# Performance work log

Hardware: AMD Instinct MI355X
Metric: run time of the kernel (lower is better)

## Reference

```python
import jax, jax.numpy as jnp
import numpy as np

L = 4          # num_layers
D = 512        # d_model
NH = 8         # num_heads
DH = 64        # d_head
DFF = 2048     # d_ff
EPS = 1e-5     # nn.LayerNorm default eps


def _layer_norm(x, g, b):
    m = x.mean(axis=-1, keepdims=True)
    v = ((x - m) ** 2).mean(axis=-1, keepdims=True)
    return (x - m) / jnp.sqrt(v + EPS) * g + b


def setup_inputs() -> dict:
    key = jax.random.key(0)
    ks = jax.random.split(key, 14)
    s = 0.02
    z = jax.random.normal(ks[0], (4, 16, D, 8, 8), dtype=jnp.float32)
    Wq = s * jax.random.normal(ks[1], (L, D, NH * DH), dtype=jnp.float32)
    Wk = s * jax.random.normal(ks[2], (L, D, NH * DH), dtype=jnp.float32)
    Wv = s * jax.random.normal(ks[3], (L, D, NH * DH), dtype=jnp.float32)
    Wo = s * jax.random.normal(ks[4], (L, NH * DH, D), dtype=jnp.float32)
    W1 = s * jax.random.normal(ks[5], (L, D, DFF), dtype=jnp.float32)
    b1 = jnp.zeros((L, DFF), dtype=jnp.float32)
    W2 = s * jax.random.normal(ks[6], (L, DFF, D), dtype=jnp.float32)
    b2 = jnp.zeros((L, D), dtype=jnp.float32)
    ln1_g = jnp.ones((L, D), dtype=jnp.float32)
    ln1_b = jnp.zeros((L, D), dtype=jnp.float32)
    ln2_g = jnp.ones((L, D), dtype=jnp.float32)
    ln2_b = jnp.zeros((L, D), dtype=jnp.float32)
    return {"z": z, "Wq": Wq, "Wk": Wk, "Wv": Wv, "Wo": Wo,
            "W1": W1, "b1": b1, "W2": W2, "b2": b2,
            "ln1_g": ln1_g, "ln1_b": ln1_b, "ln2_g": ln2_g, "ln2_b": ln2_b}


def _forward(z, Wq, Wk, Wv, Wo, W1, b1, W2, b2, ln1_g, ln1_b, ln2_g, ln2_b):
    B, T, Dm, H, W = z.shape
    N = H * W
    Tp = T * N  # T' = t*h*w
    # sinusoidal positional embedding over T' positions
    pos = jnp.arange(Tp, dtype=z.dtype)
    inv_freq = 1.0 / (10000.0 ** (jnp.arange(0, Dm, 2, dtype=z.dtype) / Dm))
    si = pos[:, None] * inv_freq[None, :]                 # (T', D/2)
    pos_emb = jnp.concatenate([jnp.sin(si), jnp.cos(si)], axis=-1)[:, None, :]  # (T',1,D)
    # rearrange 'b t d h w -> (t h w) b d'
    x = jnp.transpose(z, (1, 3, 4, 0, 2)).reshape(Tp, B, Dm)
    x = x + pos_emb
    # block-causal mask at block size N (True = masked)
    blk = jnp.arange(Tp) // N
    mask = blk[None, :] > blk[:, None]                    # (T'_q, T'_k)
    scale = 1.0 / np.sqrt(DH)
    outs = []
    for l in range(L):
        # post-lnorm multi-head attention (LN applied before residual add)
        q = (x @ Wq[l]).reshape(Tp, B, NH, DH)
        k = (x @ Wk[l]).reshape(Tp, B, NH, DH)
        v = (x @ Wv[l]).reshape(Tp, B, NH, DH)
        s = jnp.einsum('ibnd,jbnd->ijbn', q, k) * scale
        s = jnp.where(mask[:, :, None, None], -jnp.inf, s)
        p = jax.nn.softmax(s, axis=1)
        av = jnp.einsum('ijbn,jbnd->ibnd', p, v).reshape(Tp, B, NH * DH)
        attn = _layer_norm(av @ Wo[l], ln1_g[l], ln1_b[l])
        x = attn + x
        ff = _layer_norm(jax.nn.relu(x @ W1[l] + b1[l]) @ W2[l] + b2[l], ln2_g[l], ln2_b[l])
        x = ff + x
        outs.append(x)
    out = jnp.stack(outs, axis=1)                         # (T', L, B, D)
    # rearrange '(t h w) l b d -> b t l d h w'
    out = out.reshape(T, H, W, L, B, Dm)
    return jnp.transpose(out, (4, 0, 3, 5, 1, 2))


def reference(z, Wq, Wk, Wv, Wo, W1, b1, W2, b2, ln1_g, ln1_b, ln2_g, ln2_b):
    return _forward(z, Wq, Wk, Wv, Wo, W1, b1, W2, b2, ln1_g, ln1_b, ln2_g, ln2_b)
```

## Files before the change

### kernel.cpp

```cpp
#include <hip/hip_runtime.h>
#include <hip/hip_bf16.h>
#include <math.h>


#define TP 1024
#define BB 4
#define DD 512
#define DHEAD 64
#define DFF 2048
#define MROWS (TP*BB)
#define EPS 1e-5f
#define CSC 0.18033688011112042f

typedef __attribute__((ext_vector_type(8))) short bf16x8;
typedef __attribute__((ext_vector_type(4))) float f32x4;

__device__ __forceinline__ float b2f(unsigned short u) {
    union { unsigned int i; float f; } z; z.i = ((unsigned int)u) << 16; return z.f;
}
__device__ __forceinline__ unsigned short f2bu(float f) {
    __hip_bfloat16 h = __float2bfloat16(f);
    return *reinterpret_cast<unsigned short*>(&h);
}

#define WAITV0() asm volatile("s_waitcnt vmcnt(0)" ::: "memory")
#define WAITV4() asm volatile("s_waitcnt vmcnt(4)" ::: "memory")
#define WAITV8() asm volatile("s_waitcnt vmcnt(8)" ::: "memory")
#define WAITL0() asm volatile("s_waitcnt lgkmcnt(0)" ::: "memory")
__device__ __forceinline__ void hard_barrier() {
    __builtin_amdgcn_sched_barrier(0);
    __builtin_amdgcn_s_barrier();
    __builtin_amdgcn_sched_barrier(0);
}
__device__ __forceinline__ void waitv_ahead(int ahead) {
    if (ahead == 2) WAITV8();
    else if (ahead == 1) WAITV4();
    else WAITV0();
}
#define GLOAD(gp, lp) __builtin_amdgcn_global_load_lds( \
    (const __attribute__((address_space(1))) void*)(gp), \
    (__attribute__((address_space(3))) void*)(lp), 16, 0, 0)

__device__ __forceinline__ int fsw(int row) { return (row ^ (row >> 2)) & 3; }

__global__ __launch_bounds__(256) void embed_kernel(const float* __restrict__ z,
                                                    float* __restrict__ x,
                                                    __hip_bfloat16* __restrict__ x_bf) {
    __shared__ float tile[64][65];
    const int blk = blockIdx.x;
    const int dc = blk & 7, b = (blk >> 3) & 3, t = blk >> 5;
    const int tid = threadIdx.x;
#pragma unroll
    for (int it = 0; it < 4; ++it) {
        int idx = it * 256 + tid;
        int d_i = idx >> 4, hw4 = (idx & 15) * 4;
        int d = dc * 64 + d_i;
        float4 v = *reinterpret_cast<const float4*>(
            z + ((size_t)((b * 16 + t) * 512 + d)) * 64 + hw4);
        int j = d & 255;
        float freq = expf(-(float)(2 * j) * (9.210340371976184f / 512.0f));
        int i0 = t * 64 + hw4;
#pragma unroll
        for (int e = 0; e < 4; ++e) {
            float si = (float)(i0 + e) * freq;
            float pe = (d < 256) ? sinf(si) : cosf(si);
            tile[d_i][hw4 + e] = ((&v.x)[e]) + pe;
        }
    }
    __syncthreads();
#pragma unroll
    for (int it = 0; it < 4; ++it) {
        int idx = it * 256 + tid;
        int hw_o = idx >> 4, dq = (idx & 15) * 4;
        int row = (t * 64 + hw_o) * 4 + b;
        float4 v = make_float4(tile[dq][hw_o], tile[dq + 1][hw_o],
                               tile[dq + 2][hw_o], tile[dq + 3][hw_o]);
        *reinterpret_cast<float4*>(x + (size_t)row * 512 + dc * 64 + dq) = v;
        ushort4 u;
        u.x = f2bu(v.x); u.y = f2bu(v.y); u.z = f2bu(v.z); u.w = f2bu(v.w);
        *reinterpret_cast<ushort4*>((unsigned short*)x_bf + (size_t)row * 512 + dc * 64 + dq) = u;
    }
}

__global__ __launch_bounds__(256) void wt_convert(
    const float* __restrict__ Wq, const float* __restrict__ Wk,
    const float* __restrict__ Wv, const float* __restrict__ Wo,
    const float* __restrict__ W1, const float* __restrict__ W2,
    __hip_bfloat16* __restrict__ wall) {
    __shared__ float tile[32][33];
    const int l = blockIdx.y;
    __hip_bfloat16* wl = wall + (size_t)l * (4 * 512 * 512 + 2 * 512 * 2048);
    int b = blockIdx.x;
    const float* src; __hip_bfloat16* dst; int R, C, local, cbs;
    if (b < 1024) {
        int m = b >> 8; local = b & 255; R = 512; C = 512; cbs = 4;
        src = ((m == 0) ? Wq : (m == 1) ? Wk : (m == 2) ? Wv : Wo) + (size_t)l * 512 * 512;
        dst = wl + m * 512 * 512;
    } else if (b < 2048) {
        local = b - 1024; R = 512; C = 2048; cbs = 6;
        src = W1 + (size_t)l * 512 * 2048; dst = wl + 4 * 512 * 512;
    } else {
        local = b - 2048; R = 2048; C = 512; cbs = 4;
        src = W2 + (size_t)l * 2048 * 512; dst = wl + 4 * 512 * 512 + 512 * 2048;
    }
    int bx = local & ((1 << cbs) - 1), by = local >> cbs;
    int tx = threadIdx.x & 31, ty = threadIdx.x >> 5;
#pragma unroll
    for (int j = 0; j < 4; ++j)
        tile[ty + j * 8][tx] = src[(size_t)(by * 32 + ty + j * 8) * C + bx * 32 + tx];
    __syncthreads();
#pragma unroll
    for (int j = 0; j < 4; ++j)
        dst[(size_t)(bx * 32 + ty + j * 8) * R + by * 32 + tx] =
            __float2bfloat16(tile[tx][ty + j * 8]);
}

template<bool BIAS, bool RELU, bool OUT_BF16>
__global__ __launch_bounds__(256) void gemm_k(const __hip_bfloat16* __restrict__ A,
                                              const __hip_bfloat16* __restrict__ Bt,
                                              const float* __restrict__ bias,
                                              void* __restrict__ Cout,
                                              int N, int K, int ntx) {
    __shared__ __hip_bfloat16 As[4][128 * 32];
    __shared__ __hip_bfloat16 Bs[4][128 * 32];

    const int lb = blockIdx.x;
    const int wg = (lb & 7) * (gridDim.x >> 3) + (lb >> 3);
    const int m0 = (wg / ntx) * 128;
    const int n0 = (wg % ntx) * 128;

    const int tid  = threadIdx.x;
    const int wave = tid >> 6;
    const int lane = tid & 63;
    const int lr   = lane & 15;
    const int hi   = lane >> 4;
    const int lk   = (hi ^ fsw(lr)) << 3;
    const int wr   = (wave >> 1) * 64;
    const int wc   = (wave & 1) * 64;

    f32x4 acc[4][4];
#pragma unroll
    for (int i = 0; i < 4; ++i)
#pragma unroll
        for (int j = 0; j < 4; ++j) acc[i][j] = (f32x4){0.f, 0.f, 0.f, 0.f};

    const int c0 = tid, c1 = tid + 256;
    const __hip_bfloat16* a0 = A  + (size_t)(m0 + (c0 >> 2)) * K + (((c0 & 3) ^ fsw(c0 >> 2)) << 3);
    const __hip_bfloat16* a1 = A  + (size_t)(m0 + (c1 >> 2)) * K + (((c1 & 3) ^ fsw(c1 >> 2)) << 3);
    const __hip_bfloat16* b0 = Bt + (size_t)(n0 + (c0 >> 2)) * K + (((c0 & 3) ^ fsw(c0 >> 2)) << 3);
    const __hip_bfloat16* b1 = Bt + (size_t)(n0 + (c1 >> 2)) * K + (((c1 & 3) ^ fsw(c1 >> 2)) << 3);
    const int o0 = wave * 512, o1 = 2048 + wave * 512;

    const int nst = K >> 5;
#pragma unroll
    for (int s = 0; s < 3; ++s) {
        GLOAD(a0 + s * 32, &As[s][o0]); GLOAD(a1 + s * 32, &As[s][o1]);
        GLOAD(b0 + s * 32, &Bs[s][o0]); GLOAD(b1 + s * 32, &Bs[s][o1]);
    }

    for (int k = 0; k < nst; ++k) {
        const int ahead = (nst - 1 - k >= 2) ? 2 : (nst - 1 - k);
        waitv_ahead(ahead);
        hard_barrier();
        if (k + 3 < nst) {
            const int kk = (k + 3) << 5, bb = (k + 3) & 3;
            GLOAD(a0 + kk, &As[bb][o0]); GLOAD(a1 + kk, &As[bb][o1]);
            GLOAD(b0 + kk, &Bs[bb][o0]); GLOAD(b1 + kk, &Bs[bb][o1]);
        }
        const int buf = k & 3;
        bf16x8 af[4], bfv[4];
#pragma unroll
        for (int i = 0; i < 4; ++i)
            af[i] = *reinterpret_cast<const bf16x8*>(&As[buf][(size_t)(wr + i * 16 + lr) * 32 + lk]);
#pragma unroll
        for (int j = 0; j < 4; ++j)
            bfv[j] = *reinterpret_cast<const bf16x8*>(&Bs[buf][(size_t)(wc + j * 16 + lr) * 32 + lk]);
        __builtin_amdgcn_s_setprio(1);
#pragma unroll
        for (int i = 0; i < 4; ++i)
#pragma unroll
            for (int j = 0; j < 4; ++j)
                acc[i][j] = __builtin_amdgcn_mfma_f32_16x16x32_bf16(af[i], bfv[j], acc[i][j], 0, 0, 0);
        __builtin_amdgcn_s_setprio(0);
    }

#pragma unroll
    for (int j = 0; j < 4; ++j) {
        int col = n0 + wc + j * 16 + lr;
        float bv = BIAS ? bias[col] : 0.0f;
#pragma unroll
        for (int i = 0; i < 4; ++i) {
            int row = m0 + wr + i * 16 + (hi << 2);
#pragma unroll
            for (int r = 0; r < 4; ++r) {
                float v = acc[i][j][r] + bv;
                if (RELU) v = fmaxf(v, 0.0f);
                if (OUT_BF16)
                    ((unsigned short*)Cout)[(size_t)(row + r) * N + col] = f2bu(v);
                else
                    ((float*)Cout)[(size_t)(row + r) * N + col] = v;
            }
        }
    }
}

template<bool BIAS, bool RELU, int OUTMODE>
__device__ __forceinline__ void gemm64_body(const __hip_bfloat16* __restrict__ A,
                                            const __hip_bfloat16* __restrict__ Bt,
                                            const float* __restrict__ bias,
                                            void* __restrict__ Cout,
                                            unsigned short* __restrict__ vtout,
                                            int K, float scale,
                                            __hip_bfloat16* As, __hip_bfloat16* Bs) {
    const int lb = blockIdx.x;
    const int wg = (lb & 7) * (gridDim.x >> 3) + (lb >> 3);
    const int m0 = (wg >> 3) * 64;
    const int n0 = (wg & 7) * 64;

    const int tid  = threadIdx.x;
    const int wave = tid >> 6;
    const int lane = tid & 63;
    const int lr   = lane & 15;
    const int hi   = lane >> 4;
    const int wr   = (wave >> 1) * 32;
    const int wc   = (wave & 1) * 32;

    f32x4 acc[2][2];
#pragma unroll
    for (int i = 0; i < 2; ++i)
#pragma unroll
        for (int j = 0; j < 2; ++j) acc[i][j] = (f32x4){0.f, 0.f, 0.f, 0.f};

    const int c0 = tid, c1 = tid + 256;
    const __hip_bfloat16* a0 = A  + (size_t)(m0 + (c0 >> 3)) * K + (((c0 & 7) ^ ((c0 >> 3) & 7)) << 3);
    const __hip_bfloat16* a1 = A  + (size_t)(m0 + (c1 >> 3)) * K + (((c1 & 7) ^ ((c1 >> 3) & 7)) << 3);
    const __hip_bfloat16* b0 = Bt + (size_t)(n0 + (c0 >> 3)) * K + (((c0 & 7) ^ ((c0 >> 3) & 7)) << 3);
    const __hip_bfloat16* b1 = Bt + (size_t)(n0 + (c1 >> 3)) * K + (((c1 & 7) ^ ((c1 >> 3) & 7)) << 3);
    const int o0 = wave * 512, o1 = 2048 + wave * 512;

    const int nst = K >> 6;
#pragma unroll
    for (int s = 0; s < 3; ++s) {
        if (s < nst) {
            GLOAD(a0 + s * 64, As + s * 4096 + o0); GLOAD(a1 + s * 64, As + s * 4096 + o1);
            GLOAD(b0 + s * 64, Bs + s * 4096 + o0); GLOAD(b1 + s * 64, Bs + s * 4096 + o1);
        }
    }

    for (int k = 0; k < nst; ++k) {
        const int ahead = (nst - 1 - k >= 2) ? 2 : (nst - 1 - k);
        waitv_ahead(ahead);
        hard_barrier();
        if (k + 3 < nst) {
            const int kk = (k + 3) << 6;
            const int bo = ((k + 3) & 3) * 4096;
            GLOAD(a0 + kk, As + bo + o0); GLOAD(a1 + kk, As + bo + o1);
            GLOAD(b0 + kk, Bs + bo + o0); GLOAD(b1 + kk, Bs + bo + o1);
        }
        const __hip_bfloat16* Ab = As + (k & 3) * 4096;
        const __hip_bfloat16* Bb = Bs + (k & 3) * 4096;
        __builtin_amdgcn_s_setprio(1);
#pragma unroll
        for (int ks = 0; ks < 2; ++ks) {
            bf16x8 af[2], bfv[2];
#pragma unroll
            for (int i = 0; i < 2; ++i) {
                int row = wr + i * 16 + lr;
                af[i] = *reinterpret_cast<const bf16x8*>(
                    &Ab[(size_t)row * 64 + (((ks * 4 + hi) ^ (row & 7)) << 3)]);
            }
#pragma unroll
            for (int j = 0; j < 2; ++j) {
                int row = wc + j * 16 + lr;
                bfv[j] = *reinterpret_cast<const bf16x8*>(
                    &Bb[(size_t)row * 64 + (((ks * 4 + hi) ^ (row & 7)) << 3)]);
            }
#pragma unroll
            for (int i = 0; i < 2; ++i)
#pragma unroll
                for (int j = 0; j < 2; ++j)
                    acc[i][j] = __builtin_amdgcn_mfma_f32_16x16x32_bf16(af[i], bfv[j], acc[i][j], 0, 0, 0);
        }
        __builtin_amdgcn_s_setprio(0);
    }

    if (OUTMODE == 2) {
        hard_barrier();
        unsigned short* T = (unsigned short*)As;
        const int TS = 68;
#pragma unroll
        for (int j = 0; j < 2; ++j)
#pragma unroll
            for (int i = 0; i < 2; ++i)
#pragma unroll
                for (int r = 0; r < 4; ++r)
                    T[(wr + i * 16 + (hi << 2) + r) * TS + wc + j * 16 + lr] =
                        f2bu(acc[i][j][r]);
        hard_barrier();
        const int b = tid >> 6, d = tid & 63;
        const int n = n0 >> 6, t0 = m0 >> 2;
        bf16x8 v0, v1;
#pragma unroll
        for (int e = 0; e < 8; ++e) {
            v0[e] = (short)T[((e) * 4 + b) * TS + d];
            v1[e] = (short)T[((e + 8) * 4 + b) * TS + d];
        }
        unsigned short* dst = vtout + ((size_t)((b * 8 + n) * 64 + d)) * 1024 + t0;
        *reinterpret_cast<bf16x8*>(dst) = v0;
        *reinterpret_cast<bf16x8*>(dst + 8) = v1;
        return;
    }

#pragma unroll
    for (int j = 0; j < 2; ++j) {
        int col = n0 + wc + j * 16 + lr;
        float bv = BIAS ? bias[col] : 0.0f;
#pragma unroll
        for (int i = 0; i < 2; ++i) {
            int row = m0 + wr + i * 16 + (hi << 2);
#pragma unroll
            for (int r = 0; r < 4; ++r) {
                float v = acc[i][j][r] * scale + bv;
                if (RELU) v = fmaxf(v, 0.0f);
                if (OUTMODE == 1)
                    ((unsigned short*)Cout)[(size_t)(row + r) * 512 + col] = f2bu(v);
                else
                    ((float*)Cout)[(size_t)(row + r) * 512 + col] = v;
            }
        }
    }
}

template<bool BIAS, bool RELU, bool OUT_BF16>
__global__ __launch_bounds__(256) void gemm64_k(const __hip_bfloat16* __restrict__ A,
                                                const __hip_bfloat16* __restrict__ Bt,
                                                const float* __restrict__ bias,
                                                void* __restrict__ Cout, int K) {
    __shared__ __hip_bfloat16 As[4 * 64 * 64];
    __shared__ __hip_bfloat16 Bs[4 * 64 * 64];
    gemm64_body<BIAS, RELU, OUT_BF16 ? 1 : 0>(A, Bt, bias, Cout, nullptr, K, 1.0f, As, Bs);
}

__global__ __launch_bounds__(256) void qkv_out_k(const __hip_bfloat16* __restrict__ A,
                                                 const __hip_bfloat16* __restrict__ B0,
                                                 const __hip_bfloat16* __restrict__ B1,
                                                 const __hip_bfloat16* __restrict__ B2,
                                                 __hip_bfloat16* __restrict__ C0,
                                                 __hip_bfloat16* __restrict__ C1,
                                                 unsigned short* __restrict__ vt,
                                                 const float* __restrict__ x,
                                                 float* __restrict__ out, int outl) {
    __shared__ __hip_bfloat16 As[4 * 64 * 64];
    __shared__ __hip_bfloat16 Bs[4 * 64 * 64];
    const int sel = blockIdx.z;
    if (sel == 3) {
        float (*tile)[65] = reinterpret_cast<float(*)[65]>(As);
        const int blk = blockIdx.x;
        const int dc = blk & 7;
        const int b  = (blk >> 3) & 3;
        const int t  = blk >> 5;
        const int tid = threadIdx.x;
#pragma unroll
        for (int it = 0; it < 4; ++it) {
            int c = tid + it * 256;
            int hw = c >> 4, f4 = c & 15;
            const float* src = x + (size_t)((t * 64 + hw) * 4 + b) * 512 + dc * 64 + f4 * 4;
            float4 v = *reinterpret_cast<const float4*>(src);
            tile[hw][f4 * 4 + 0] = v.x; tile[hw][f4 * 4 + 1] = v.y;
            tile[hw][f4 * 4 + 2] = v.z; tile[hw][f4 * 4 + 3] = v.w;
        }
        __syncthreads();
        size_t ob = (((size_t)(b * 16 + t) * 4 + outl) * 512 + dc * 64) * 64;
#pragma unroll
        for (int it = 0; it < 4; ++it) {
            int c = tid + it * 256;
            int d = c >> 4, f4 = c & 15;
            float4 v = make_float4(tile[f4 * 4 + 0][d], tile[f4 * 4 + 1][d],
                                   tile[f4 * 4 + 2][d], tile[f4 * 4 + 3][d]);
            *reinterpret_cast<float4*>(out + ob + (size_t)d * 64 + f4 * 4) = v;
        }
        return;
    }
    if (sel == 2) {
        gemm64_body<false, false, 2>(A, B2, nullptr, nullptr, vt, 512, 1.0f, As, Bs);
    } else if (sel == 1) {
        gemm64_body<false, false, 1>(A, B1, nullptr, (void*)C1, nullptr, 512, 1.0f, As, Bs);
    } else {
        gemm64_body<false, false, 1>(A, B0, nullptr, (void*)C0, nullptr, 512, CSC, As, Bs);
    }
}

__device__ __forceinline__ int aswz(int row, int col) {
    return (row * 64 + col) ^ ((row & 7) << 3);
}

__device__ __forceinline__ void stage_tile(const unsigned short* gbase, int stride,
                                           unsigned short* lds, int wave, int tid) {
#pragma unroll
    for (int it = 0; it < 2; ++it) {
        int c = tid + it * 256;
        int row = c >> 3;
        int i = (c & 7) ^ (row & 7);
        const unsigned short* g = gbase + (size_t)row * stride + i * 8;
        __builtin_amdgcn_global_load_lds(
            (const __attribute__((address_space(1))) void*)g,
            (__attribute__((address_space(3))) void*)(lds + it * 2048 + wave * 512),
            16, 0, 0);
    }
}

__global__ __launch_bounds__(256) void attn_mfma(const unsigned short* __restrict__ q,
                                                 const unsigned short* __restrict__ k,
                                                 const unsigned short* __restrict__ vt,
                                                 unsigned short* __restrict__ av) {
    __shared__ unsigned short Qs[64 * 64];
    __shared__ unsigned short Ks[4][64 * 64];
    __shared__ unsigned short Vts[4][64 * 64];
    __shared__ unsigned short Ps[64 * 64];

    const int tid = threadIdx.x;
    const int wave = tid >> 6, lane = tid & 63;
    const int lr = lane & 15, hi = lane >> 4;
    const int wr = wave * 16;

    const int p = blockIdx.x;
    const int xcd = p & 7, idx = p >> 3;
    const int bn = xcd * 4 + (idx & 3);
    const int qb = 15 - (idx >> 2);
    const int b = bn >> 3, n = bn & 7;

    const unsigned short* kcol  = k  + (size_t)b * 512 + n * 64;
    const unsigned short* vtrow = vt + (size_t)(bn * 64) * 1024;

    stage_tile(q + ((size_t)(qb * 64) * 4 + b) * 512 + n * 64, 2048, Qs, wave, tid);
    stage_tile(kcol, 2048, Ks[0], wave, tid);
    stage_tile(vtrow, 1024, Vts[0], wave, tid);
    if (qb >= 1) {
        stage_tile(kcol + (size_t)64 * 2048, 2048, Ks[1], wave, tid);
        stage_tile(vtrow + 64, 1024, Vts[1], wave, tid);
    }
    if (qb >= 2) {
        stage_tile(kcol + (size_t)128 * 2048, 2048, Ks[2], wave, tid);
        stage_tile(vtrow + 128, 1024, Vts[2], wave, tid);
    }

    f32x4 o_acc[4], l_acc;
#pragma unroll
    for (int db = 0; db < 4; ++db) o_acc[db] = (f32x4){0.f, 0.f, 0.f, 0.f};
    l_acc = (f32x4){0.f, 0.f, 0.f, 0.f};

    bf16x8 onesf;
#pragma unroll
    for (int e = 0; e < 8; ++e) onesf[e] = (short)0x3F80;

    bf16x8 qf[2];

    for (int kb = 0; kb <= qb; ++kb) {
        const int ahead = (qb - kb >= 2) ? 2 : (qb - kb);
        waitv_ahead(ahead);
        hard_barrier();
        if (kb + 3 <= qb) {
            stage_tile(kcol + (size_t)(kb + 3) * 64 * 2048, 2048,
                       Ks[(kb + 3) & 3], wave, tid);
            stage_tile(vtrow + (kb + 3) * 64, 1024, Vts[(kb + 3) & 3], wave, tid);
        }
        if (kb == 0) {
#pragma unroll
            for (int ks = 0; ks < 2; ++ks)
                qf[ks] = *reinterpret_cast<const bf16x8*>(
                    (const unsigned short*)Qs + aswz(wr + lr, ks * 32 + hi * 8));
        }
        const unsigned short* Kb = Ks[kb & 3];
        const unsigned short* Vb = Vts[kb & 3];

        f32x4 sf[4];
#pragma unroll
        for (int jb = 0; jb < 4; ++jb) sf[jb] = (f32x4){0.f, 0.f, 0.f, 0.f};
        __builtin_amdgcn_s_setprio(1);
#pragma unroll
        for (int ks = 0; ks < 2; ++ks) {
            bf16x8 a = qf[ks];
#pragma unroll
            for (int jb = 0; jb < 4; ++jb) {
                bf16x8 kf = *reinterpret_cast<const bf16x8*>(
                    Kb + aswz(jb * 16 + lr, ks * 32 + hi * 8));
                sf[jb] = __builtin_amdgcn_mfma_f32_16x16x32_bf16(a, kf, sf[jb], 0, 0, 0);
            }
        }
        __builtin_amdgcn_s_setprio(0);

#pragma unroll
        for (int jb = 0; jb < 4; ++jb)
#pragma unroll
            for (int r = 0; r < 4; ++r) {
                float pe = exp2f(fminf(sf[jb][r], 100.0f));
                Ps[aswz(wr + 4 * hi + r, jb * 16 + lr)] = f2bu(pe);
            }
        WAITL0();
        hard_barrier();

        __builtin_amdgcn_s_setprio(1);
#pragma unroll
        for (int ks = 0; ks < 2; ++ks) {
            bf16x8 pf = *reinterpret_cast<const bf16x8*>(
                (const unsigned short*)Ps + aswz(wr + lr, ks * 32 + hi * 8));
            l_acc = __builtin_amdgcn_mfma_f32_16x16x32_bf16(pf, onesf, l_acc, 0, 0, 0);
#pragma unroll
            for (int db = 0; db < 4; ++db) {
                bf16x8 vf = *reinterpret_cast<const bf16x8*>(
                    Vb + aswz(db * 16 + lr, ks * 32 + hi * 8));
                o_acc[db] = __builtin_amdgcn_mfma_f32_16x16x32_bf16(pf, vf, o_acc[db], 0, 0, 0);
            }
        }
        __builtin_amdgcn_s_setprio(0);
    }

#pragma unroll
    for (int r = 0; r < 4; ++r) {
        float inv = 1.0f / l_acc[r];
        int row = qb * 64 + wr + 4 * hi + r;
#pragma unroll
        for (int db = 0; db < 4; ++db)
            av[((size_t)row * 4 + b) * 512 + n * 64 + db * 16 + lr] =
                f2bu(o_acc[db][r] * inv);
    }
}

__global__ __launch_bounds__(64) void add_ln_kernel(const float* __restrict__ y,
                                                    const float* __restrict__ g,
                                                    const float* __restrict__ bta,
                                                    float* __restrict__ x,
                                                    __hip_bfloat16* __restrict__ x_bf) {
    const int row = blockIdx.x;
    const int tid = threadIdx.x;
    const float* yr = y + (size_t)row * DD;
    float4 v0 = *reinterpret_cast<const float4*>(&yr[tid * 4]);
    float4 v1 = *reinterpret_cast<const float4*>(&yr[256 + tid * 4]);
    float s = v0.x + v0.y + v0.z + v0.w + v1.x + v1.y + v1.z + v1.w;
    float ss = v0.x * v0.x + v0.y * v0.y + v0.z * v0.z + v0.w * v0.w +
               v1.x * v1.x + v1.y * v1.y + v1.z * v1.z + v1.w * v1.w;
#pragma unroll
    for (int off = 32; off; off >>= 1) {
        s  += __shfl_xor(s, off);
        ss += __shfl_xor(ss, off);
    }
    float mean = s * (1.0f / 512.0f);
    float var = ss * (1.0f / 512.0f) - mean * mean;
    float rstd = rsqrtf(var + EPS);

    float* xr = x + (size_t)row * DD;
    float vals[8] = {v0.x, v0.y, v0.z, v0.w, v1.x, v1.y, v1.z, v1.w};
#pragma unroll
    for (int e = 0; e < 8; ++e) {
        int d = (e < 4) ? (tid * 4 + e) : (256 + tid * 4 + (e - 4));
        float nrm = (vals[e] - mean) * rstd * g[d] + bta[d];
        float xo = xr[d] + nrm;
        xr[d] = xo;
        x_bf[(size_t)row * DD + d] = __float2bfloat16(xo);
    }
}

__global__ __launch_bounds__(256) void out_transpose(const float* __restrict__ x,
                                                     float* __restrict__ out, int l) {
    __shared__ float tile[64][65];
    const int blk = blockIdx.x;
    const int dc = blk & 7;
    const int b  = (blk >> 3) & 3;
    const int t  = blk >> 5;
    const int tid = threadIdx.x;
#pragma unroll
    for (int it = 0; it < 4; ++it) {
        int c = tid + it * 256;
        int hw = c >> 4, f4 = c & 15;
        const float* src = x + (size_t)((t * 64 + hw) * 4 + b) * 512 + dc * 64 + f4 * 4;
        float4 v = *reinterpret_cast<const float4*>(src);
        tile[hw][f4 * 4 + 0] = v.x; tile[hw][f4 * 4 + 1] = v.y;
        tile[hw][f4 * 4 + 2] = v.z; tile[hw][f4 * 4 + 3] = v.w;
    }
    __syncthreads();
    size_t ob = (((size_t)(b * 16 + t) * 4 + l) * 512 + dc * 64) * 64;
#pragma unroll
    for (int it = 0; it < 4; ++it) {
        int c = tid + it * 256;
        int d = c >> 4, f4 = c & 15;
        float4 v = make_float4(tile[f4 * 4 + 0][d], tile[f4 * 4 + 1][d],
                               tile[f4 * 4 + 2][d], tile[f4 * 4 + 3][d]);
        *reinterpret_cast<float4*>(out + ob + (size_t)d * 64 + f4 * 4) = v;
    }
}

extern "C" void kernel_launch(void* const* d_in, const int* in_sizes, int n_in,
                              void* d_out, int out_size, void* d_ws, size_t ws_size,
                              hipStream_t stream) {
    const float* z    = (const float*)d_in[0];
    const float* Wq   = (const float*)d_in[1];
    const float* Wk   = (const float*)d_in[2];
    const float* Wv   = (const float*)d_in[3];
    const float* Wo   = (const float*)d_in[4];
    const float* W1   = (const float*)d_in[5];
    const float* b1   = (const float*)d_in[6];
    const float* W2   = (const float*)d_in[7];
    const float* b2   = (const float*)d_in[8];
    const float* ln1g = (const float*)d_in[9];
    const float* ln1b = (const float*)d_in[10];
    const float* ln2g = (const float*)d_in[11];
    const float* ln2b = (const float*)d_in[12];
    float* out = (float*)d_out;

    const size_t MB = 1u << 20;
    char* base = (char*)d_ws;
    float*          x     = (float*)(base);
    __hip_bfloat16* x_bf  = (__hip_bfloat16*)(base + 8  * MB);
    __hip_bfloat16* q_bf  = (__hip_bfloat16*)(base + 12 * MB);
    __hip_bfloat16* k_bf  = (__hip_bfloat16*)(base + 16 * MB);
    __hip_bfloat16* av_bf = (__hip_bfloat16*)(base + 24 * MB);
    float*          tmp   = (float*)(base + 28 * MB);
    __hip_bfloat16* wall  = (__hip_bfloat16*)(base + 36 * MB);
    __hip_bfloat16* ff1_bf = q_bf;
    unsigned short* vt    = (unsigned short*)(base + 20 * MB);

    const size_t WL = 4 * 512 * 512 + 2 * 512 * 2048;

    embed_kernel<<<512, 256, 0, stream>>>(z, x, x_bf);
    wt_convert<<<dim3(3072, 4), 256, 0, stream>>>(Wq, Wk, Wv, Wo, W1, W2, wall);

    for (int l = 0; l < 4; ++l) {
        __hip_bfloat16* wl  = wall + (size_t)l * WL;
        __hip_bfloat16* wqt = wl;
        __hip_bfloat16* wkt = wqt + 512 * 512;
        __hip_bfloat16* wvt = wkt + 512 * 512;
        __hip_bfloat16* wot = wvt + 512 * 512;
        __hip_bfloat16* w1t = wot + 512 * 512;
        __hip_bfloat16* w2t = w1t + 512 * 2048;

        qkv_out_k<<<dim3(512, 1, l == 0 ? 3 : 4), 256, 0, stream>>>(
            x_bf, wqt, wkt, wvt, q_bf, k_bf, vt, x, out, l - 1);

        attn_mfma<<<512, 256, 0, stream>>>(
            (const unsigned short*)q_bf, (const unsigned short*)k_bf,
            vt, (unsigned short*)av_bf);

        gemm64_k<false, false, false><<<512, 256, 0, stream>>>(
            av_bf, wot, nullptr, (void*)tmp, 512);
        add_ln_kernel<<<MROWS, 64, 0, stream>>>(tmp, ln1g + l * 512, ln1b + l * 512,
                                                x, x_bf);

        gemm_k<true, true, true><<<512, 256, 0, stream>>>(
            x_bf, w1t, b1 + l * 2048, (void*)ff1_bf, 2048, 512, 16);
        gemm64_k<true, false, false><<<512, 256, 0, stream>>>(
            ff1_bf, w2t, b2 + l * 512, (void*)tmp, 2048);
        add_ln_kernel<<<MROWS, 64, 0, stream>>>(tmp, ln2g + l * 512, ln2b + l * 512,
                                                x, x_bf);
    }
    out_transpose<<<512, 256, 0, stream>>>(x, out, 3);
}
```

Before: 419.0 us.

## Use split-K 128x128 GEMM for Wo/W2 and fuse partial-sum reduction into LayerNorm

```diff
diff --git a/kernel.cpp b/kernel.cpp
--- a/kernel.cpp
+++ b/kernel.cpp
@@ -204,6 +204,96 @@
     }
 }
 
+template<bool OUT1F32>
+__global__ __launch_bounds__(256) void gemm_ks(const __hip_bfloat16* __restrict__ A,
+                                               const __hip_bfloat16* __restrict__ Bt,
+                                               float* __restrict__ out0,
+                                               void* __restrict__ out1,
+                                               int Kstr, int Klen) {
+    __shared__ __hip_bfloat16 As[4][128 * 32];
+    __shared__ __hip_bfloat16 Bs[4][128 * 32];
+
+    const int lb = blockIdx.x;
+    const int wg = (lb & 7) * 32 + (lb >> 3);
+    const int slice = wg >> 7;
+    const int tile  = wg & 127;
+    const int m0 = (tile >> 2) * 128;
+    const int n0 = (tile & 3) * 128;
+    const int koff = slice * Klen;
+
+    const int tid  = threadIdx.x;
+    const int wave = tid >> 6;
+    const int lane = tid & 63;
+    const int lr   = lane & 15;
+    const int hi   = lane >> 4;
+    const int lk   = (hi ^ fsw(lr)) << 3;
+    const int wr   = (wave >> 1) * 64;
+    const int wc   = (wave & 1) * 64;
+
+    f32x4 acc[4][4];
+#pragma unroll
+    for (int i = 0; i < 4; ++i)
+#pragma unroll
+        for (int j = 0; j < 4; ++j) acc[i][j] = (f32x4){0.f, 0.f, 0.f, 0.f};
+
+    const int c0 = tid, c1 = tid + 256;
+    const __hip_bfloat16* a0 = A  + (size_t)(m0 + (c0 >> 2)) * Kstr + koff + (((c0 & 3) ^ fsw(c0 >> 2)) << 3);
+    const __hip_bfloat16* a1 = A  + (size_t)(m0 + (c1 >> 2)) * Kstr + koff + (((c1 & 3) ^ fsw(c1 >> 2)) << 3);
+    const __hip_bfloat16* b0 = Bt + (size_t)(n0 + (c0 >> 2)) * Kstr + koff + (((c0 & 3) ^ fsw(c0 >> 2)) << 3);
+    const __hip_bfloat16* b1 = Bt + (size_t)(n0 + (c1 >> 2)) * Kstr + koff + (((c1 & 3) ^ fsw(c1 >> 2)) << 3);
+    const int o0 = wave * 512, o1 = 2048 + wave * 512;
+
+    const int nst = Klen >> 5;
+#pragma unroll
+    for (int s = 0; s < 3; ++s) {
+        GLOAD(a0 + s * 32, &As[s][o0]); GLOAD(a1 + s * 32, &As[s][o1]);
+        GLOAD(b0 + s * 32, &Bs[s][o0]); GLOAD(b1 + s * 32, &Bs[s][o1]);
+    }
+
+    for (int k = 0; k < nst; ++k) {
+        const int ahead = (nst - 1 - k >= 2) ? 2 : (nst - 1 - k);
+        waitv_ahead(ahead);
+        hard_barrier();
+        if (k + 3 < nst) {
+            const int kk = (k + 3) << 5, bb = (k + 3) & 3;
+            GLOAD(a0 + kk, &As[bb][o0]); GLOAD(a1 + kk, &As[bb][o1]);
+            GLOAD(b0 + kk, &Bs[bb][o0]); GLOAD(b1 + kk, &Bs[bb][o1]);
+        }
+        const int buf = k & 3;
+        bf16x8 af[4], bfv[4];
+#pragma unroll
+        for (int i = 0; i < 4; ++i)
+            af[i] = *reinterpret_cast<const bf16x8*>(&As[buf][(size_t)(wr + i * 16 + lr) * 32 + lk]);
+#pragma unroll
+        for (int j = 0; j < 4; ++j)
+            bfv[j] = *reinterpret_cast<const bf16x8*>(&Bs[buf][(size_t)(wc + j * 16 + lr) * 32 + lk]);
+        __builtin_amdgcn_s_setprio(1);
+#pragma unroll
+        for (int i = 0; i < 4; ++i)
+#pragma unroll
+            for (int j = 0; j < 4; ++j)
+                acc[i][j] = __builtin_amdgcn_mfma_f32_16x16x32_bf16(af[i], bfv[j], acc[i][j], 0, 0, 0);
+        __builtin_amdgcn_s_setprio(0);
+    }
+
+#pragma unroll
+    for (int j = 0; j < 4; ++j) {
+        int col = n0 + wc + j * 16 + lr;
+#pragma unroll
+        for (int i = 0; i < 4; ++i) {
+            int row = m0 + wr + i * 16 + (hi << 2);
+#pragma unroll
+            for (int r = 0; r < 4; ++r) {
+                float v = acc[i][j][r];
+                size_t off = (size_t)(row + r) * 512 + col;
+                if (slice == 0) out0[off] = v;
+                else if (OUT1F32) ((float*)out1)[off] = v;
+                else ((unsigned short*)out1)[off] = f2bu(v);
+            }
+        }
+    }
+}
+
 template<bool BIAS, bool RELU, int OUTMODE>
 __device__ __forceinline__ void gemm64_body(const __hip_bfloat16* __restrict__ A,
                                             const __hip_bfloat16* __restrict__ Bt,
@@ -329,16 +419,6 @@
             }
         }
     }
-}
-
-template<bool BIAS, bool RELU, bool OUT_BF16>
-__global__ __launch_bounds__(256) void gemm64_k(const __hip_bfloat16* __restrict__ A,
-                                                const __hip_bfloat16* __restrict__ Bt,
-                                                const float* __restrict__ bias,
-                                                void* __restrict__ Cout, int K) {
-    __shared__ __hip_bfloat16 As[4 * 64 * 64];
-    __shared__ __hip_bfloat16 Bs[4 * 64 * 64];
-    gemm64_body<BIAS, RELU, OUT_BF16 ? 1 : 0>(A, Bt, bias, Cout, nullptr, K, 1.0f, As, Bs);
 }
 
 __global__ __launch_bounds__(256) void qkv_out_k(const __hip_bfloat16* __restrict__ A,
@@ -526,37 +606,65 @@
     }
 }
 
-__global__ __launch_bounds__(64) void add_ln_kernel(const float* __restrict__ y,
-                                                    const float* __restrict__ g,
-                                                    const float* __restrict__ bta,
-                                                    float* __restrict__ x,
-                                                    __hip_bfloat16* __restrict__ x_bf) {
-    const int row = blockIdx.x;
-    const int tid = threadIdx.x;
-    const float* yr = y + (size_t)row * DD;
-    float4 v0 = *reinterpret_cast<const float4*>(&yr[tid * 4]);
-    float4 v1 = *reinterpret_cast<const float4*>(&yr[256 + tid * 4]);
-    float s = v0.x + v0.y + v0.z + v0.w + v1.x + v1.y + v1.z + v1.w;
-    float ss = v0.x * v0.x + v0.y * v0.y + v0.z * v0.z + v0.w * v0.w +
-               v1.x * v1.x + v1.y * v1.y + v1.z * v1.z + v1.w * v1.w;
-#pragma unroll
-    for (int off = 32; off; off >>= 1) {
-        s  += __shfl_xor(s, off);
-        ss += __shfl_xor(ss, off);
-    }
-    float mean = s * (1.0f / 512.0f);
-    float var = ss * (1.0f / 512.0f) - mean * mean;
-    float rstd = rsqrtf(var + EPS);
-
-    float* xr = x + (size_t)row * DD;
-    float vals[8] = {v0.x, v0.y, v0.z, v0.w, v1.x, v1.y, v1.z, v1.w};
-#pragma unroll
-    for (int e = 0; e < 8; ++e) {
-        int d = (e < 4) ? (tid * 4 + e) : (256 + tid * 4 + (e - 4));
-        float nrm = (vals[e] - mean) * rstd * g[d] + bta[d];
-        float xo = xr[d] + nrm;
-        xr[d] = xo;
-        x_bf[(size_t)row * DD + d] = __float2bfloat16(xo);
+__global__ __launch_bounds__(256) void add_ln_kernel(const float* __restrict__ s0,
+                                                     const float* __restrict__ s1f,
+                                                     const unsigned short* __restrict__ s1b,
+                                                     const float* __restrict__ bias,
+                                                     const float* __restrict__ g,
+                                                     const float* __restrict__ beta,
+                                                     float* __restrict__ x,
+                                                     __hip_bfloat16* __restrict__ x_bf) {
+    const int wid = threadIdx.x >> 6, lane = threadIdx.x & 63;
+#pragma unroll
+    for (int p = 0; p < 2; ++p) {
+        const int row = blockIdx.x * 8 + wid * 2 + p;
+        const int d0 = lane * 8;
+        float y[8];
+        float4 a0 = *reinterpret_cast<const float4*>(s0 + (size_t)row * 512 + d0);
+        float4 a1 = *reinterpret_cast<const float4*>(s0 + (size_t)row * 512 + d0 + 4);
+        y[0] = a0.x; y[1] = a0.y; y[2] = a0.z; y[3] = a0.w;
+        y[4] = a1.x; y[5] = a1.y; y[6] = a1.z; y[7] = a1.w;
+        if (s1f) {
+            float4 c0 = *reinterpret_cast<const float4*>(s1f + (size_t)row * 512 + d0);
+            float4 c1 = *reinterpret_cast<const float4*>(s1f + (size_t)row * 512 + d0 + 4);
+            y[0] += c0.x; y[1] += c0.y; y[2] += c0.z; y[3] += c0.w;
+            y[4] += c1.x; y[5] += c1.y; y[6] += c1.z; y[7] += c1.w;
+        }
+        if (s1b) {
+            ushort4 u0 = *reinterpret_cast<const ushort4*>(s1b + (size_t)row * 512 + d0);
+            ushort4 u1 = *reinterpret_cast<const ushort4*>(s1b + (size_t)row * 512 + d0 + 4);
+            y[0] += b2f(u0.x); y[1] += b2f(u0.y); y[2] += b2f(u0.z); y[3] += b2f(u0.w);
+            y[4] += b2f(u1.x); y[5] += b2f(u1.y); y[6] += b2f(u1.z); y[7] += b2f(u1.w);
+        }
+        if (bias) {
+#pragma unroll
+            for (int e = 0; e < 8; ++e) y[e] += bias[d0 + e];
+        }
+        float s = 0.f, ss = 0.f;
+#pragma unroll
+        for (int e = 0; e < 8; ++e) { s += y[e]; ss += y[e] * y[e]; }
+#pragma unroll
+        for (int off = 32; off; off >>= 1) {
+            s  += __shfl_xor(s, off);
+            ss += __shfl_xor(ss, off);
+        }
+        float mean = s * (1.0f / 512.0f);
+        float var = ss * (1.0f / 512.0f) - mean * mean;
+        float rstd = rsqrtf(var + EPS);
+
+        float* xr = x + (size_t)row * 512 + d0;
+        unsigned short* xbr = (unsigned short*)x_bf + (size_t)row * 512 + d0;
+        float xo[8];
+#pragma unroll
+        for (int e = 0; e < 8; ++e)
+            xo[e] = (y[e] - mean) * rstd * g[d0 + e] + beta[d0 + e] + xr[e];
+        *reinterpret_cast<float4*>(xr)     = make_float4(xo[0], xo[1], xo[2], xo[3]);
+        *reinterpret_cast<float4*>(xr + 4) = make_float4(xo[4], xo[5], xo[6], xo[7]);
+        ushort4 o0, o1;
+        o0.x = f2bu(xo[0]); o0.y = f2bu(xo[1]); o0.z = f2bu(xo[2]); o0.w = f2bu(xo[3]);
+        o1.x = f2bu(xo[4]); o1.y = f2bu(xo[5]); o1.z = f2bu(xo[6]); o1.w = f2bu(xo[7]);
+        *reinterpret_cast<ushort4*>(xbr)     = o0;
+        *reinterpret_cast<ushort4*>(xbr + 4) = o1;
     }
 }
 
@@ -613,11 +721,13 @@
     __hip_bfloat16* x_bf  = (__hip_bfloat16*)(base + 8  * MB);
     __hip_bfloat16* q_bf  = (__hip_bfloat16*)(base + 12 * MB);
     __hip_bfloat16* k_bf  = (__hip_bfloat16*)(base + 16 * MB);
+    unsigned short* vt    = (unsigned short*)(base + 20 * MB);
     __hip_bfloat16* av_bf = (__hip_bfloat16*)(base + 24 * MB);
     float*          tmp   = (float*)(base + 28 * MB);
     __hip_bfloat16* wall  = (__hip_bfloat16*)(base + 36 * MB);
     __hip_bfloat16* ff1_bf = q_bf;
-    unsigned short* vt    = (unsigned short*)(base + 20 * MB);
+    float*          woslc1 = (float*)(base + 12 * MB);
+    unsigned short* ffslc1 = (unsigned short*)(base + 24 * MB);
 
     const size_t WL = 4 * 512 * 512 + 2 * 512 * 2048;
 
@@ -640,17 +750,18 @@
             (const unsigned short*)q_bf, (const unsigned short*)k_bf,
             vt, (unsigned short*)av_bf);
 
-        gemm64_k<false, false, false><<<512, 256, 0, stream>>>(
-            av_bf, wot, nullptr, (void*)tmp, 512);
-        add_ln_kernel<<<MROWS, 64, 0, stream>>>(tmp, ln1g + l * 512, ln1b + l * 512,
-                                                x, x_bf);
+        gemm_ks<true><<<256, 256, 0, stream>>>(av_bf, wot, tmp, (void*)woslc1,
+                                               512, 256);
+        add_ln_kernel<<<512, 256, 0, stream>>>(tmp, woslc1, nullptr, nullptr,
+                                               ln1g + l * 512, ln1b + l * 512, x, x_bf);
 
         gemm_k<true, true, true><<<512, 256, 0, stream>>>(
             x_bf, w1t, b1 + l * 2048, (void*)ff1_bf, 2048, 512, 16);
-        gemm64_k<true, false, false><<<512, 256, 0, stream>>>(
-            ff1_bf, w2t, b2 + l * 512, (void*)tmp, 2048);
-        add_ln_kernel<<<MROWS, 64, 0, stream>>>(tmp, ln2g + l * 512, ln2b + l * 512,
-                                                x, x_bf);
+
+        gemm_ks<false><<<256, 256, 0, stream>>>(ff1_bf, w2t, tmp, (void*)ffslc1,
+                                                2048, 1024);
+        add_ln_kernel<<<512, 256, 0, stream>>>(tmp, nullptr, ffslc1, b2 + l * 512,
+                                               ln2g + l * 512, ln2b + l * 512, x, x_bf);
     }
     out_transpose<<<512, 256, 0, stream>>>(x, out, 3);
 }
```

Measured after the change: 493.7 us. 17.8% more time.
